# Kernel tuning notes

Hardware: AMD Instinct MI355X
Metric: run time of the kernel (lower is better)

## Reference

```python
import jax, jax.numpy as jnp
import numpy as np

L, B, D = 1024, 24, 512


def setup_inputs() -> dict:
    key = jax.random.key(0)
    ks = jax.random.split(key, 9)
    s = 1.0 / np.sqrt(D)
    return {
        "v": jax.random.normal(ks[0], (L, B, D), dtype=jnp.float32),
        "h0": jax.random.normal(ks[1], (B, D), dtype=jnp.float32),
        "V": jax.random.normal(ks[2], (B, D), dtype=jnp.float32),
        "Wp": jax.random.normal(ks[3], (D, D), dtype=jnp.float32) * s,
        "Wp_": jax.random.normal(ks[4], (D, D), dtype=jnp.float32) * s,
        "w_ih": jax.random.normal(ks[5], (3 * D, D), dtype=jnp.float32) * s,
        "w_hh": jax.random.normal(ks[6], (3 * D, D), dtype=jnp.float32) * s,
        "b_ih": jax.random.normal(ks[7], (3 * D,), dtype=jnp.float32) * s,
        "b_hh": jax.random.normal(ks[8], (3 * D,), dtype=jnp.float32) * s,
    }


def reference(v, h0, V, Wp, Wp_, w_ih, w_hh, b_ih, b_hh):
    # v: [l, b, d]. Precompute both projections once (original wastefully
    # recomputes Wp_(v) per step; the math is identical).
    Wpv_all = jnp.einsum('lbd,hd->lbh', v, Wp)    # per-step query proj
    Wpvp = jnp.einsum('lbd,hd->lbh', v, Wp_)      # shared key proj

    def step(h, wpv_i):
        # additive attention over all l positions
        x = jnp.tanh(wpv_i[None, :, :] + Wpvp)           # [l, b, h]
        s = jnp.einsum('lbh,bh->bl', x, V)               # scores
        a = jax.nn.softmax(s, axis=1)                    # [b, l]
        c = jnp.einsum('bl,lbd->bd', a, v)               # context [b, d]
        # torch.nn.GRUCell math
        gi = c @ w_ih.T + b_ih
        gh = h @ w_hh.T + b_hh
        i_r, i_z, i_n = jnp.split(gi, 3, axis=1)
        h_r, h_z, h_n = jnp.split(gh, 3, axis=1)
        r = jax.nn.sigmoid(i_r + h_r)
        z = jax.nn.sigmoid(i_z + h_z)
        n = jnp.tanh(i_n + r * h_n)
        h_new = (1.0 - z) * n + z * h
        return h_new, h_new

    _, hs = jax.lax.scan(step, h0, Wpv_all)              # hs: [l, b, d]
    # dropout is identity in eval mode
    return hs
```

## Files before the change

### kernel.cpp

```cpp
#include <hip/hip_runtime.h>
#include <math.h>


#define GRU_FLAG_STRIDE 32

__launch_bounds__(256, 2)
__global__ void gemm_abt_kernel(const float* __restrict__ A, const float* __restrict__ B,
                                float* __restrict__ out, int K, int N,
                                const float* __restrict__ bias, int do_tanh) {
  __shared__ __align__(16) float As[16][136];
  __shared__ __align__(16) float Bs[16][136];
  const int m0 = blockIdx.y * 128, n0 = blockIdx.x * 128;
  const int tid = threadIdx.x;
  const int tm = (tid & 15) * 8, tn = (tid >> 4) * 8;
  const int srow = tid & 127, scol = (tid >> 7) * 8;
  const float* Ap = A + (size_t)(m0 + srow) * K + scol;
  const float* Bp = B + (size_t)(n0 + srow) * K + scol;
  float acc[8][8] = {{0.f}};
  for (int k0 = 0; k0 < K; k0 += 16) {
    const float4 a0 = *(const float4*)(Ap + k0);
    const float4 a1 = *(const float4*)(Ap + k0 + 4);
    const float4 b0 = *(const float4*)(Bp + k0);
    const float4 b1 = *(const float4*)(Bp + k0 + 4);
    __syncthreads();
    As[scol + 0][srow] = a0.x; As[scol + 1][srow] = a0.y;
    As[scol + 2][srow] = a0.z; As[scol + 3][srow] = a0.w;
    As[scol + 4][srow] = a1.x; As[scol + 5][srow] = a1.y;
    As[scol + 6][srow] = a1.z; As[scol + 7][srow] = a1.w;
    Bs[scol + 0][srow] = b0.x; Bs[scol + 1][srow] = b0.y;
    Bs[scol + 2][srow] = b0.z; Bs[scol + 3][srow] = b0.w;
    Bs[scol + 4][srow] = b1.x; Bs[scol + 5][srow] = b1.y;
    Bs[scol + 6][srow] = b1.z; Bs[scol + 7][srow] = b1.w;
    __syncthreads();
#pragma unroll
    for (int kk = 0; kk < 16; ++kk) {
      const float4 av0 = *(const float4*)&As[kk][tm];
      const float4 av1 = *(const float4*)&As[kk][tm + 4];
      const float4 bv0 = *(const float4*)&Bs[kk][tn];
      const float4 bv1 = *(const float4*)&Bs[kk][tn + 4];
      const float ar[8] = {av0.x, av0.y, av0.z, av0.w, av1.x, av1.y, av1.z, av1.w};
      const float br[8] = {bv0.x, bv0.y, bv0.z, bv0.w, bv1.x, bv1.y, bv1.z, bv1.w};
#pragma unroll
      for (int r = 0; r < 8; ++r)
#pragma unroll
        for (int c = 0; c < 8; ++c)
          acc[r][c] = fmaf(ar[r], br[c], acc[r][c]);
    }
  }
#pragma unroll
  for (int r = 0; r < 8; ++r) {
    float* o = out + (size_t)(m0 + tm + r) * N + n0 + tn;
#pragma unroll
    for (int c = 0; c < 8; ++c) {
      float val = acc[r][c];
      if (bias) val += bias[n0 + tn + c];
      if (do_tanh) val = tanhf(val);
      o[c] = val;
    }
  }
}

__launch_bounds__(256, 3)
__global__ void attn_kernel(const float* __restrict__ tq, const float* __restrict__ tk,
                            const float* __restrict__ Vv, const float* __restrict__ v,
                            float* __restrict__ Cout) {
  const int b = blockIdx.y;
  const int it = blockIdx.x;
  const int tid = threadIdx.x;
  const int wave = tid >> 6, lane = tid & 63;
  const int h8 = lane * 8;
  __shared__ __align__(16) float sm[4][1024];
  __shared__ __align__(16) float red[4][4][512];
  __shared__ float inv_s[4];

  float q[4][8], vp[4][8];
  {
    const float* vvp = Vv + (size_t)b * 512 + h8;
    const float4 v0 = *(const float4*)vvp;
    const float4 v1 = *(const float4*)(vvp + 4);
    const float vv[8] = {v0.x, v0.y, v0.z, v0.w, v1.x, v1.y, v1.z, v1.w};
#pragma unroll
    for (int ii = 0; ii < 4; ++ii) {
      const float* qp = tq + ((size_t)(it * 4 + ii) * 24 + b) * 512 + h8;
      const float4 q0 = *(const float4*)qp;
      const float4 q1 = *(const float4*)(qp + 4);
      q[ii][0] = q0.x; q[ii][1] = q0.y; q[ii][2] = q0.z; q[ii][3] = q0.w;
      q[ii][4] = q1.x; q[ii][5] = q1.y; q[ii][6] = q1.z; q[ii][7] = q1.w;
#pragma unroll
      for (int j = 0; j < 8; ++j)
        vp[ii][j] = vv[j] * (1.0f - q[ii][j] * q[ii][j]);
    }
  }

  for (int l = wave; l < 1024; l += 4) {
    const float* kp = tk + ((size_t)l * 24 + b) * 512 + h8;
    const float4 k0 = *(const float4*)kp;
    const float4 k1 = *(const float4*)(kp + 4);
    const float kkv[8] = {k0.x, k0.y, k0.z, k0.w, k1.x, k1.y, k1.z, k1.w};
    float acc0 = 0.f, acc1 = 0.f, acc2 = 0.f, acc3 = 0.f;
#pragma unroll
    for (int j = 0; j < 8; ++j) {
      const float w = kkv[j];
      acc0 = fmaf(vp[0][j] * w, __builtin_amdgcn_rcpf(fmaf(q[0][j], w, 1.0f)), acc0);
      acc1 = fmaf(vp[1][j] * w, __builtin_amdgcn_rcpf(fmaf(q[1][j], w, 1.0f)), acc1);
      acc2 = fmaf(vp[2][j] * w, __builtin_amdgcn_rcpf(fmaf(q[2][j], w, 1.0f)), acc2);
      acc3 = fmaf(vp[3][j] * w, __builtin_amdgcn_rcpf(fmaf(q[3][j], w, 1.0f)), acc3);
    }
#pragma unroll
    for (int mask = 32; mask; mask >>= 1) {
      acc0 += __shfl_xor(acc0, mask, 64);
      acc1 += __shfl_xor(acc1, mask, 64);
      acc2 += __shfl_xor(acc2, mask, 64);
      acc3 += __shfl_xor(acc3, mask, 64);
    }
    if (lane == 0) {
      sm[0][l] = acc0; sm[1][l] = acc1; sm[2][l] = acc2; sm[3][l] = acc3;
    }
  }
  __syncthreads();

  {
    float* row = sm[wave];
    float m = -1e30f;
    for (int t = lane; t < 1024; t += 64) m = fmaxf(m, row[t]);
#pragma unroll
    for (int mask = 32; mask; mask >>= 1) m = fmaxf(m, __shfl_xor(m, mask, 64));
    float s = 0.f;
    for (int t = lane; t < 1024; t += 64) {
      const float e = __expf(row[t] - m);
      row[t] = e;
      s += e;
    }
#pragma unroll
    for (int mask = 32; mask; mask >>= 1) s += __shfl_xor(s, mask, 64);
    if (lane == 0) inv_s[wave] = 1.0f / s;
  }
  __syncthreads();

  float ca[4][8] = {{0.f}};
  const int l0 = wave * 256;
  for (int l = l0; l < l0 + 256; ++l) {
    const float* vrow = v + ((size_t)l * 24 + b) * 512 + h8;
    const float4 x0 = *(const float4*)vrow;
    const float4 x1 = *(const float4*)(vrow + 4);
    const float a0 = sm[0][l], a1 = sm[1][l], a2 = sm[2][l], a3 = sm[3][l];
    const float xv[8] = {x0.x, x0.y, x0.z, x0.w, x1.x, x1.y, x1.z, x1.w};
#pragma unroll
    for (int j = 0; j < 8; ++j) {
      ca[0][j] = fmaf(a0, xv[j], ca[0][j]);
      ca[1][j] = fmaf(a1, xv[j], ca[1][j]);
      ca[2][j] = fmaf(a2, xv[j], ca[2][j]);
      ca[3][j] = fmaf(a3, xv[j], ca[3][j]);
    }
  }
#pragma unroll
  for (int ii = 0; ii < 4; ++ii) {
    *(float4*)&red[wave][ii][h8]     = make_float4(ca[ii][0], ca[ii][1], ca[ii][2], ca[ii][3]);
    *(float4*)&red[wave][ii][h8 + 4] = make_float4(ca[ii][4], ca[ii][5], ca[ii][6], ca[ii][7]);
  }
  __syncthreads();
  {
    const int ii = tid >> 6;
    const int d0 = (tid & 63) * 8;
    float4 s0 = *(const float4*)&red[0][ii][d0];
    float4 s1 = *(const float4*)&red[0][ii][d0 + 4];
#pragma unroll
    for (int w = 1; w < 4; ++w) {
      const float4 r0 = *(const float4*)&red[w][ii][d0];
      const float4 r1 = *(const float4*)&red[w][ii][d0 + 4];
      s0.x += r0.x; s0.y += r0.y; s0.z += r0.z; s0.w += r0.w;
      s1.x += r1.x; s1.y += r1.y; s1.z += r1.z; s1.w += r1.w;
    }
    const float inv = inv_s[ii];
    s0.x *= inv; s0.y *= inv; s0.z *= inv; s0.w *= inv;
    s1.x *= inv; s1.y *= inv; s1.z *= inv; s1.w *= inv;
    float* o = Cout + ((size_t)(it * 4 + ii) * 24 + b) * 512 + d0;
    *(float4*)o = s0;
    *(float4*)(o + 4) = s1;
  }
}

__launch_bounds__(512, 1)
__global__ void gru_persist_kernel(const float* __restrict__ Gi_c, const float* __restrict__ w_hh,
                                   const float* __restrict__ b_hh, const float* __restrict__ h0,
                                   float* __restrict__ hb0, float* __restrict__ hb1,
                                   float* __restrict__ out, unsigned* __restrict__ flags,
                                   int gstep0) {
  const int bg = blockIdx.x % 24;
  const int sl = blockIdx.x / 24;
  const int t = threadIdx.x;
  const int d_loc = t & 63;
  const int kc = t >> 6;
  const int dglob = sl * 64 + d_loc;

  __shared__ __align__(16) float h_lds[512];
  __shared__ float red[3][64][9];
  __shared__ float ghs[3][64];

  float wreg[3][64];
#pragma unroll
  for (int g = 0; g < 3; ++g) {
    const float* wr = w_hh + (size_t)(g * 512 + dglob) * 512 + kc * 64;
#pragma unroll
    for (int j = 0; j < 64; j += 4) {
      const float4 wv = *(const float4*)(wr + j);
      wreg[g][j] = wv.x; wreg[g][j + 1] = wv.y; wreg[g][j + 2] = wv.z; wreg[g][j + 3] = wv.w;
    }
  }
  const float bias_r = b_hh[dglob];
  const float bias_z = b_hh[512 + dglob];
  const float bias_n = b_hh[1024 + dglob];

  unsigned* myflags = flags + (size_t)bg * 8 * GRU_FLAG_STRIDE;

  for (int il = 0; il < 128; ++il) {
    const int gs = gstep0 + il;
    if (t < 8) {
      while (__hip_atomic_load(&myflags[t * GRU_FLAG_STRIDE], __ATOMIC_RELAXED,
                               __HIP_MEMORY_SCOPE_AGENT) < (unsigned)gs) {
        __builtin_amdgcn_s_sleep(2);
      }
    }
    __syncthreads();

    const float* hsrc = (gs == 0) ? (h0 + (size_t)bg * 512)
                                  : (((gs & 1) ? hb0 : hb1) + (size_t)bg * 512);
    if (t < 256) {
      const unsigned long long u = __hip_atomic_load(
          (const unsigned long long*)hsrc + t, __ATOMIC_RELAXED, __HIP_MEMORY_SCOPE_AGENT);
      union { unsigned long long u; float f[2]; } cv; cv.u = u;
      h_lds[2 * t] = cv.f[0];
      h_lds[2 * t + 1] = cv.f[1];
    }

    float gir = 0.f, giz = 0.f, gin = 0.f;
    if (t < 64) {
      const float* gi = Gi_c + ((size_t)il * 24 + bg) * 1536;
      gir = gi[dglob]; giz = gi[512 + dglob]; gin = gi[1024 + dglob];
    }
    __syncthreads();

    float a0 = 0.f, a1 = 0.f, a2 = 0.f, b0 = 0.f, b1 = 0.f, b2 = 0.f;
#pragma unroll
    for (int j = 0; j < 64; j += 8) {
      const float4 h1 = *(const float4*)&h_lds[kc * 64 + j];
      const float4 h2 = *(const float4*)&h_lds[kc * 64 + j + 4];
      a0 = fmaf(h1.x, wreg[0][j], fmaf(h1.y, wreg[0][j+1], fmaf(h1.z, wreg[0][j+2], fmaf(h1.w, wreg[0][j+3], a0))));
      b0 = fmaf(h2.x, wreg[0][j+4], fmaf(h2.y, wreg[0][j+5], fmaf(h2.z, wreg[0][j+6], fmaf(h2.w, wreg[0][j+7], b0))));
      a1 = fmaf(h1.x, wreg[1][j], fmaf(h1.y, wreg[1][j+1], fmaf(h1.z, wreg[1][j+2], fmaf(h1.w, wreg[1][j+3], a1))));
      b1 = fmaf(h2.x, wreg[1][j+4], fmaf(h2.y, wreg[1][j+5], fmaf(h2.z, wreg[1][j+6], fmaf(h2.w, wreg[1][j+7], b1))));
      a2 = fmaf(h1.x, wreg[2][j], fmaf(h1.y, wreg[2][j+1], fmaf(h1.z, wreg[2][j+2], fmaf(h1.w, wreg[2][j+3], a2))));
      b2 = fmaf(h2.x, wreg[2][j+4], fmaf(h2.y, wreg[2][j+5], fmaf(h2.z, wreg[2][j+6], fmaf(h2.w, wreg[2][j+7], b2))));
    }
    red[0][d_loc][kc] = a0 + b0;
    red[1][d_loc][kc] = a1 + b1;
    red[2][d_loc][kc] = a2 + b2;
    __syncthreads();

    if (t < 192) {
      const int g = t >> 6, d = t & 63;
      const float* rr = red[g][d];
      ghs[g][d] = ((rr[0] + rr[1]) + (rr[2] + rr[3])) + ((rr[4] + rr[5]) + (rr[6] + rr[7]));
    }
    __syncthreads();

    if (t < 64) {
      const float hold = h_lds[dglob];
      const float r = 1.0f / (1.0f + __expf(-(gir + ghs[0][t] + bias_r)));
      const float z = 1.0f / (1.0f + __expf(-(giz + ghs[1][t] + bias_z)));
      const float n = tanhf(gin + r * (ghs[2][t] + bias_n));
      const float hn = (1.0f - z) * n + z * hold;
      float* hdst = ((gs & 1) ? hb1 : hb0) + (size_t)bg * 512;
      __hip_atomic_store(&hdst[dglob], hn, __ATOMIC_RELAXED, __HIP_MEMORY_SCOPE_AGENT);
      out[((size_t)gs * 24 + bg) * 512 + dglob] = hn;
      if (t == 0) {
        __hip_atomic_store(&myflags[sl * GRU_FLAG_STRIDE], (unsigned)(gs + 1),
                           __ATOMIC_RELEASE, __HIP_MEMORY_SCOPE_AGENT);
      }
    }
    __syncthreads();
  }
}

extern "C" void kernel_launch(void* const* d_in, const int* in_sizes, int n_in,
                              void* d_out, int out_size, void* d_ws, size_t ws_size,
                              hipStream_t stream) {
  (void)in_sizes; (void)n_in; (void)out_size;
  const float* v    = (const float*)d_in[0];
  const float* h0   = (const float*)d_in[1];
  const float* Vv   = (const float*)d_in[2];
  const float* Wp   = (const float*)d_in[3];
  const float* Wp_  = (const float*)d_in[4];
  const float* w_ih = (const float*)d_in[5];
  const float* w_hh = (const float*)d_in[6];
  const float* b_ih = (const float*)d_in[7];
  const float* b_hh = (const float*)d_in[8];
  float* out = (float*)d_out;

  const bool full_tq = ws_size >= (size_t)125927500;
  float* ws   = (float*)d_ws;
  float* tk   = ws;
  float* tqF  = tk + (size_t)12582912;
  float* tq_c = tk + (size_t)12582912;
  float* C_c  = full_tq ? (tqF + (size_t)12582912) : (tq_c + (size_t)1572864);
  float* Gi_c = C_c + (size_t)1572864;
  float* hb0  = Gi_c + (size_t)4718592;
  float* hb1  = hb0 + (size_t)12288;
  unsigned* flags = (unsigned*)(hb1 + (size_t)12288);

  hipMemsetAsync(flags, 0, (size_t)24 * 8 * GRU_FLAG_STRIDE * sizeof(unsigned), stream);

  gemm_abt_kernel<<<dim3(4, 192), 256, 0, stream>>>(v, Wp_, tk, 512, 512, nullptr, 1);
  if (full_tq)
    gemm_abt_kernel<<<dim3(4, 192), 256, 0, stream>>>(v, Wp, tqF, 512, 512, nullptr, 1);

  for (int c = 0; c < 8; ++c) {
    const float* v_chunk = v + (size_t)c * 128 * 24 * 512;
    const float* tq_use;
    if (full_tq) {
      tq_use = tqF + (size_t)c * 128 * 24 * 512;
    } else {
      gemm_abt_kernel<<<dim3(4, 24), 256, 0, stream>>>(v_chunk, Wp, tq_c, 512, 512, nullptr, 1);
      tq_use = tq_c;
    }
    attn_kernel<<<dim3(32, 24), 256, 0, stream>>>(tq_use, tk, Vv, v, C_c);
    gemm_abt_kernel<<<dim3(12, 24), 256, 0, stream>>>(C_c, w_ih, Gi_c, 512, 1536, b_ih, 0);
    gru_persist_kernel<<<192, 512, 0, stream>>>(Gi_c, w_hh, b_hh, h0, hb0, hb1,
                                                out, flags, c * 128);
  }
}
```

Before: 7.887 ms.

## Replace GRU flag barriers with tagged h values and batch three rows per block

The persistent GRU kernel drops the separate per-slice flag array and its spin-wait barrier. Each hidden value is now stored as a 64-bit float+step-tag pair, so consumers poll the data itself and the next row's load is prefetched early. Each block now handles three batch rows with 8 slices (64 blocks instead of 192) and keeps the old h in registers. Gate math uses fast rcp and exp-based tanh. This removes the flag round trip and a barrier per step, but serialises three rows per block and loosens numerical accuracy slightly.

```diff
diff --git a/kernel.cpp b/kernel.cpp
--- a/kernel.cpp
+++ b/kernel.cpp
@@ -1,8 +1,6 @@
 #include <hip/hip_runtime.h>
 #include <math.h>
 
-
-#define GRU_FLAG_STRIDE 32
 
 __launch_bounds__(256, 2)
 __global__ void gemm_abt_kernel(const float* __restrict__ A, const float* __restrict__ B,
@@ -180,14 +178,21 @@
   }
 }
 
+union HPack {
+  unsigned long long u;
+  struct { float f; unsigned tag; } s;
+};
+
 __launch_bounds__(512, 1)
-__global__ void gru_persist_kernel(const float* __restrict__ Gi_c, const float* __restrict__ w_hh,
-                                   const float* __restrict__ b_hh, const float* __restrict__ h0,
-                                   float* __restrict__ hb0, float* __restrict__ hb1,
-                                   float* __restrict__ out, unsigned* __restrict__ flags,
-                                   int gstep0) {
-  const int bg = blockIdx.x % 24;
-  const int sl = blockIdx.x / 24;
+__global__ void gru_persist_kernel(const float* __restrict__ Gi_c,
+                                   const float* __restrict__ w_hh,
+                                   const float* __restrict__ b_hh,
+                                   const float* __restrict__ h0,
+                                   unsigned long long* __restrict__ hb0,
+                                   unsigned long long* __restrict__ hb1,
+                                   float* __restrict__ out, int gstep0) {
+  const int g  = blockIdx.x & 7;
+  const int sl = blockIdx.x >> 3;
   const int t = threadIdx.x;
   const int d_loc = t & 63;
   const int kc = t >> 6;
@@ -195,90 +200,102 @@
 
   __shared__ __align__(16) float h_lds[512];
   __shared__ float red[3][64][9];
-  __shared__ float ghs[3][64];
 
   float wreg[3][64];
 #pragma unroll
-  for (int g = 0; g < 3; ++g) {
-    const float* wr = w_hh + (size_t)(g * 512 + dglob) * 512 + kc * 64;
+  for (int gg = 0; gg < 3; ++gg) {
+    const float* wr = w_hh + (size_t)(gg * 512 + dglob) * 512 + kc * 64;
 #pragma unroll
     for (int j = 0; j < 64; j += 4) {
       const float4 wv = *(const float4*)(wr + j);
-      wreg[g][j] = wv.x; wreg[g][j + 1] = wv.y; wreg[g][j + 2] = wv.z; wreg[g][j + 3] = wv.w;
+      wreg[gg][j] = wv.x; wreg[gg][j + 1] = wv.y; wreg[gg][j + 2] = wv.z; wreg[gg][j + 3] = wv.w;
     }
   }
   const float bias_r = b_hh[dglob];
   const float bias_z = b_hh[512 + dglob];
   const float bias_n = b_hh[1024 + dglob];
 
-  unsigned* myflags = flags + (size_t)bg * 8 * GRU_FLAG_STRIDE;
+  if (gstep0 == 0 && t < 192) {
+    const int q = t >> 6, d = t & 63;
+    const int bg = g * 3 + q;
+    HPack p;
+    p.s.f = h0[(size_t)bg * 512 + sl * 64 + d];
+    p.s.tag = 1u;
+    __hip_atomic_store(hb1 + (size_t)bg * 512 + sl * 64 + d, p.u,
+                       __ATOMIC_RELAXED, __HIP_MEMORY_SCOPE_AGENT);
+  }
+
+  float hq[3];
+  HPack pf;
+  pf.u = __hip_atomic_load(((gstep0 & 1) ? hb0 : hb1) + (size_t)(g * 3) * 512 + t,
+                           __ATOMIC_RELAXED, __HIP_MEMORY_SCOPE_AGENT);
 
   for (int il = 0; il < 128; ++il) {
     const int gs = gstep0 + il;
-    if (t < 8) {
-      while (__hip_atomic_load(&myflags[t * GRU_FLAG_STRIDE], __ATOMIC_RELAXED,
-                               __HIP_MEMORY_SCOPE_AGENT) < (unsigned)gs) {
-        __builtin_amdgcn_s_sleep(2);
-      }
-    }
-    __syncthreads();
-
-    const float* hsrc = (gs == 0) ? (h0 + (size_t)bg * 512)
-                                  : (((gs & 1) ? hb0 : hb1) + (size_t)bg * 512);
-    if (t < 256) {
-      const unsigned long long u = __hip_atomic_load(
-          (const unsigned long long*)hsrc + t, __ATOMIC_RELAXED, __HIP_MEMORY_SCOPE_AGENT);
-      union { unsigned long long u; float f[2]; } cv; cv.u = u;
-      h_lds[2 * t] = cv.f[0];
-      h_lds[2 * t + 1] = cv.f[1];
-    }
-
-    float gir = 0.f, giz = 0.f, gin = 0.f;
-    if (t < 64) {
-      const float* gi = Gi_c + ((size_t)il * 24 + bg) * 1536;
-      gir = gi[dglob]; giz = gi[512 + dglob]; gin = gi[1024 + dglob];
-    }
-    __syncthreads();
-
-    float a0 = 0.f, a1 = 0.f, a2 = 0.f, b0 = 0.f, b1 = 0.f, b2 = 0.f;
-#pragma unroll
-    for (int j = 0; j < 64; j += 8) {
-      const float4 h1 = *(const float4*)&h_lds[kc * 64 + j];
-      const float4 h2 = *(const float4*)&h_lds[kc * 64 + j + 4];
-      a0 = fmaf(h1.x, wreg[0][j], fmaf(h1.y, wreg[0][j+1], fmaf(h1.z, wreg[0][j+2], fmaf(h1.w, wreg[0][j+3], a0))));
-      b0 = fmaf(h2.x, wreg[0][j+4], fmaf(h2.y, wreg[0][j+5], fmaf(h2.z, wreg[0][j+6], fmaf(h2.w, wreg[0][j+7], b0))));
-      a1 = fmaf(h1.x, wreg[1][j], fmaf(h1.y, wreg[1][j+1], fmaf(h1.z, wreg[1][j+2], fmaf(h1.w, wreg[1][j+3], a1))));
-      b1 = fmaf(h2.x, wreg[1][j+4], fmaf(h2.y, wreg[1][j+5], fmaf(h2.z, wreg[1][j+6], fmaf(h2.w, wreg[1][j+7], b1))));
-      a2 = fmaf(h1.x, wreg[2][j], fmaf(h1.y, wreg[2][j+1], fmaf(h1.z, wreg[2][j+2], fmaf(h1.w, wreg[2][j+3], a2))));
-      b2 = fmaf(h2.x, wreg[2][j+4], fmaf(h2.y, wreg[2][j+5], fmaf(h2.z, wreg[2][j+6], fmaf(h2.w, wreg[2][j+7], b2))));
-    }
-    red[0][d_loc][kc] = a0 + b0;
-    red[1][d_loc][kc] = a1 + b1;
-    red[2][d_loc][kc] = a2 + b2;
-    __syncthreads();
-
-    if (t < 192) {
-      const int g = t >> 6, d = t & 63;
-      const float* rr = red[g][d];
-      ghs[g][d] = ((rr[0] + rr[1]) + (rr[2] + rr[3])) + ((rr[4] + rr[5]) + (rr[6] + rr[7]));
-    }
-    __syncthreads();
-
-    if (t < 64) {
-      const float hold = h_lds[dglob];
-      const float r = 1.0f / (1.0f + __expf(-(gir + ghs[0][t] + bias_r)));
-      const float z = 1.0f / (1.0f + __expf(-(giz + ghs[1][t] + bias_z)));
-      const float n = tanhf(gin + r * (ghs[2][t] + bias_n));
-      const float hn = (1.0f - z) * n + z * hold;
-      float* hdst = ((gs & 1) ? hb1 : hb0) + (size_t)bg * 512;
-      __hip_atomic_store(&hdst[dglob], hn, __ATOMIC_RELAXED, __HIP_MEMORY_SCOPE_AGENT);
-      out[((size_t)gs * 24 + bg) * 512 + dglob] = hn;
-      if (t == 0) {
-        __hip_atomic_store(&myflags[sl * GRU_FLAG_STRIDE], (unsigned)(gs + 1),
-                           __ATOMIC_RELEASE, __HIP_MEMORY_SCOPE_AGENT);
-      }
-    }
-    __syncthreads();
+#pragma unroll
+    for (int q = 0; q < 3; ++q) {
+      const int bg = g * 3 + q;
+      const unsigned want = (unsigned)(gs + 1);
+      const unsigned long long* src = ((gs & 1) ? hb0 : hb1) + (size_t)bg * 512 + t;
+
+      HPack p = pf;
+      {
+        const int gs_n = (q == 2) ? gs + 1 : gs;
+        const int bg_n = (q == 2) ? g * 3 : bg + 1;
+        pf.u = __hip_atomic_load(((gs_n & 1) ? hb0 : hb1) + (size_t)bg_n * 512 + t,
+                                 __ATOMIC_RELAXED, __HIP_MEMORY_SCOPE_AGENT);
+      }
+      while (p.s.tag < want) {
+        __builtin_amdgcn_s_sleep(1);
+        p.u = __hip_atomic_load(src, __ATOMIC_RELAXED, __HIP_MEMORY_SCOPE_AGENT);
+      }
+      h_lds[t] = p.s.f;
+
+      float gir = 0.f, giz = 0.f, gin = 0.f;
+      if (t < 64) {
+        const float* gi = Gi_c + ((size_t)il * 24 + bg) * 1536;
+        gir = gi[dglob]; giz = gi[512 + dglob]; gin = gi[1024 + dglob];
+      }
+      __syncthreads();
+      if (il == 0 && t < 64) hq[q] = h_lds[dglob];
+
+      float a0 = 0.f, a1 = 0.f, a2 = 0.f, b0 = 0.f, b1 = 0.f, b2 = 0.f;
+#pragma unroll
+      for (int j = 0; j < 64; j += 8) {
+        const float4 h1 = *(const float4*)&h_lds[kc * 64 + j];
+        const float4 h2 = *(const float4*)&h_lds[kc * 64 + j + 4];
+        a0 = fmaf(h1.x, wreg[0][j], fmaf(h1.y, wreg[0][j+1], fmaf(h1.z, wreg[0][j+2], fmaf(h1.w, wreg[0][j+3], a0))));
+        b0 = fmaf(h2.x, wreg[0][j+4], fmaf(h2.y, wreg[0][j+5], fmaf(h2.z, wreg[0][j+6], fmaf(h2.w, wreg[0][j+7], b0))));
+        a1 = fmaf(h1.x, wreg[1][j], fmaf(h1.y, wreg[1][j+1], fmaf(h1.z, wreg[1][j+2], fmaf(h1.w, wreg[1][j+3], a1))));
+        b1 = fmaf(h2.x, wreg[1][j+4], fmaf(h2.y, wreg[1][j+5], fmaf(h2.z, wreg[1][j+6], fmaf(h2.w, wreg[1][j+7], b1))));
+        a2 = fmaf(h1.x, wreg[2][j], fmaf(h1.y, wreg[2][j+1], fmaf(h1.z, wreg[2][j+2], fmaf(h1.w, wreg[2][j+3], a2))));
+        b2 = fmaf(h2.x, wreg[2][j+4], fmaf(h2.y, wreg[2][j+5], fmaf(h2.z, wreg[2][j+6], fmaf(h2.w, wreg[2][j+7], b2))));
+      }
+      red[0][d_loc][kc] = a0 + b0;
+      red[1][d_loc][kc] = a1 + b1;
+      red[2][d_loc][kc] = a2 + b2;
+      __syncthreads();
+
+      if (t < 64) {
+        const float* r0 = red[0][t];
+        const float* r1 = red[1][t];
+        const float* r2 = red[2][t];
+        const float sr = ((r0[0] + r0[1]) + (r0[2] + r0[3])) + ((r0[4] + r0[5]) + (r0[6] + r0[7]));
+        const float sz = ((r1[0] + r1[1]) + (r1[2] + r1[3])) + ((r1[4] + r1[5]) + (r1[6] + r1[7]));
+        const float sn = ((r2[0] + r2[1]) + (r2[2] + r2[3])) + ((r2[4] + r2[5]) + (r2[6] + r2[7]));
+        const float r = __builtin_amdgcn_rcpf(1.0f + __expf(-(gir + sr + bias_r)));
+        const float z = __builtin_amdgcn_rcpf(1.0f + __expf(-(giz + sz + bias_z)));
+        const float nx = gin + r * (sn + bias_n);
+        const float e2 = __expf(-2.0f * fabsf(nx));
+        const float tn = __builtin_copysignf((1.0f - e2) * __builtin_amdgcn_rcpf(1.0f + e2), nx);
+        const float hn = (1.0f - z) * tn + z * hq[q];
+        hq[q] = hn;
+        HPack pw; pw.s.f = hn; pw.s.tag = (unsigned)(gs + 2);
+        __hip_atomic_store(((gs & 1) ? hb1 : hb0) + (size_t)bg * 512 + dglob, pw.u,
+                           __ATOMIC_RELAXED, __HIP_MEMORY_SCOPE_AGENT);
+        out[((size_t)gs * 24 + bg) * 512 + dglob] = hn;
+      }
+    }
   }
 }
 
@@ -297,18 +314,17 @@
   const float* b_hh = (const float*)d_in[8];
   float* out = (float*)d_out;
 
-  const bool full_tq = ws_size >= (size_t)125927500;
+  const bool full_tq = ws_size >= (size_t)126025728;
   float* ws   = (float*)d_ws;
   float* tk   = ws;
   float* tqF  = tk + (size_t)12582912;
   float* tq_c = tk + (size_t)12582912;
   float* C_c  = full_tq ? (tqF + (size_t)12582912) : (tq_c + (size_t)1572864);
   float* Gi_c = C_c + (size_t)1572864;
-  float* hb0  = Gi_c + (size_t)4718592;
-  float* hb1  = hb0 + (size_t)12288;
-  unsigned* flags = (unsigned*)(hb1 + (size_t)12288);
-
-  hipMemsetAsync(flags, 0, (size_t)24 * 8 * GRU_FLAG_STRIDE * sizeof(unsigned), stream);
+  unsigned long long* hb0 = (unsigned long long*)(Gi_c + (size_t)4718592);
+  unsigned long long* hb1 = hb0 + (size_t)12288;
+
+  hipMemsetAsync(hb0, 0, (size_t)2 * 12288 * sizeof(unsigned long long), stream);
 
   gemm_abt_kernel<<<dim3(4, 192), 256, 0, stream>>>(v, Wp_, tk, 512, 512, nullptr, 1);
   if (full_tq)
@@ -325,7 +341,7 @@
     }
     attn_kernel<<<dim3(32, 24), 256, 0, stream>>>(tq_use, tk, Vv, v, C_c);
     gemm_abt_kernel<<<dim3(12, 24), 256, 0, stream>>>(C_c, w_ih, Gi_c, 512, 1536, b_ih, 0);
-    gru_persist_kernel<<<192, 512, 0, stream>>>(Gi_c, w_hh, b_hh, h0, hb0, hb1,
-                                                out, flags, c * 128);
+    gru_persist_kernel<<<64, 512, 0, stream>>>(Gi_c, w_hh, b_hh, h0, hb0, hb1,
+                                               out, c * 128);
   }
 }
```

After: 8.118 ms. +2.9%, slower.
